# Kernel tuning notes

Measured on AMD Instinct MI355X. Metric: run time of the kernel, lower is better.

## Reference

```python
import jax, jax.numpy as jnp
import numpy as np

B, N, D, H, PSI = 8, 7225, 256, 8, 64
DH = D // H
DF = 4 * D
EPS = 1e-5


def _ln(x, g, b):
    m = jnp.mean(x, axis=-1, keepdims=True)
    v = jnp.mean((x - m) ** 2, axis=-1, keepdims=True)
    return (x - m) / jnp.sqrt(v + EPS) * g + b


def _gelu(x):
    return jax.nn.gelu(x, approximate=False)


def setup_inputs() -> dict:
    key = jax.random.key(0)
    ks = jax.random.split(key, 16)
    w = lambda k, s: (jax.random.normal(k, s, dtype=jnp.float32) * 0.02)
    inp = {
        'x': jax.random.normal(ks[0], (B, N, D), dtype=jnp.float32),
        'fx': jax.random.normal(ks[1], (B, N, D), dtype=jnp.float32),
        'ln1_g': jnp.ones((D,), jnp.float32), 'ln1_b': jnp.zeros((D,), jnp.float32),
        'Wq': w(ks[2], (D, D)), 'Wk': w(ks[3], (D, D)), 'Wv': w(ks[4], (D, D)),
        'Wo': w(ks[5], (D, D)), 'bo': jnp.zeros((D,), jnp.float32),
        'ln2_g': jnp.ones((D,), jnp.float32), 'ln2_b': jnp.zeros((D,), jnp.float32),
        'mlp_W1': w(ks[6], (D, DF)), 'mlp_b1': jnp.zeros((DF,), jnp.float32),
        'mlp_W2': w(ks[7], (DF, D)), 'mlp_b2': jnp.zeros((D,), jnp.float32),
        'proj_W1': w(ks[8], (D, D)), 'proj_b1': jnp.zeros((D,), jnp.float32),
        'proj_W2': w(ks[9], (D, PSI)), 'proj_b2': jnp.zeros((PSI,), jnp.float32),
        'mu': jnp.zeros((PSI,), jnp.float32),
        'ln3_g': jnp.ones((D,), jnp.float32), 'ln3_b': jnp.zeros((D,), jnp.float32),
        'mlp2_W1': w(ks[10], (D, DF)), 'mlp2_b1': jnp.zeros((DF,), jnp.float32),
        'mlp2_W2': w(ks[11], (DF, D)), 'mlp2_b2': jnp.zeros((D,), jnp.float32),
    }
    return inp


def _forward(x, fx, ln1_g, ln1_b, Wq, Wk, Wv, Wo, bo, ln2_g, ln2_b,
             mlp_W1, mlp_b1, mlp_W2, mlp_b2, proj_W1, proj_b1, proj_W2, proj_b2,
             mu, ln3_g, ln3_b, mlp2_W1, mlp2_b1, mlp2_W2, mlp2_b2):
    # --- linear (kernelized, non-causal) self-attention ---
    h = _ln(x, ln1_g, ln1_b)
    to_heads = lambda t: t.reshape(B, N, H, DH).transpose(0, 2, 1, 3)  # bhnd
    q = to_heads(h @ Wq)
    k = to_heads(h @ Wk)
    v = to_heads(h @ Wv)
    q = jax.nn.softmax(q, axis=-1) * (DH ** -0.5)   # feature-dim softmax
    k = jax.nn.softmax(k, axis=-2)                  # sequence-dim softmax
    ctx = jnp.einsum('bhnd,bhne->bhde', k, v)       # [B,H,DH,DH]
    attn = jnp.einsum('bhnd,bhde->bhne', q, ctx)    # [B,H,N,DH]
    attn = attn.transpose(0, 2, 1, 3).reshape(B, N, D) @ Wo + bo
    x = attn + x

    # --- MLP block (n_layers=0, no residual inside MLP) ---
    h = _ln(x, ln2_g, ln2_b)
    x = _gelu(h @ mlp_W1 + mlp_b1) @ mlp_W2 + mlp_b2 + x

    # --- low-rank projection + covariance whitening (orth=True, training path) ---
    x_ = _gelu(x @ proj_W1 + proj_b1) @ proj_W2 + proj_b2       # [B,N,PSI]
    cov = jnp.einsum('blc,bld->cd', x_, x_) / (B * N)           # [PSI,PSI]
    L = jnp.linalg.cholesky(cov)
    L_inv_T = jnp.linalg.inv(L).T
    x_ = x_ @ L_inv_T

    # --- softplus-scaled low-rank operator on fx ---
    ctx2 = jnp.einsum('blp,bld->bpd', x_, fx)                   # [B,PSI,D]
    fx = jnp.einsum('blp,bpd->bld', x_ * jax.nn.softplus(mu), ctx2)

    fx = _gelu(_ln(fx, ln3_g, ln3_b) @ mlp2_W1 + mlp2_b1) @ mlp2_W2 + mlp2_b2
    return x, fx


def reference(x, fx, ln1_g, ln1_b, Wq, Wk, Wv, Wo, bo, ln2_g, ln2_b,
              mlp_W1, mlp_b1, mlp_W2, mlp_b2, proj_W1, proj_b1, proj_W2, proj_b2,
              mu, ln3_g, ln3_b, mlp2_W1, mlp2_b1, mlp2_W2, mlp2_b2):
    return _forward(x, fx, ln1_g, ln1_b, Wq, Wk, Wv, Wo, bo, ln2_g, ln2_b,
                    mlp_W1, mlp_b1, mlp_W2, mlp_b2, proj_W1, proj_b1, proj_W2, proj_b2,
                    mu, ln3_g, ln3_b, mlp2_W1, mlp2_b1, mlp2_W2, mlp2_b2)
```

## Files before the change

kernel.cpp:

```cpp
#include <hip/hip_runtime.h>
#include <math.h>

typedef unsigned short u16;
typedef unsigned int u32;
typedef float f32x4 __attribute__((ext_vector_type(4)));
typedef __bf16 bf16x8 __attribute__((ext_vector_type(8)));

#define NTOK 57800
#define NSEQ 7225
#define NBATCH 8

static __device__ __forceinline__ float bf2f(u16 u){ u32 x=((u32)u)<<16; float f; __builtin_memcpy(&f,&x,4); return f; }
static __device__ __forceinline__ u16 f2bf(float f){ __bf16 h = (__bf16)f; u16 u; __builtin_memcpy(&u,&h,2); return u; }
static __device__ __forceinline__ float gelu_f(float v){
  float t = v * v;
  float w = fmaf(t, -0.07135481627f, -1.5957691216f);
  float e = __expf(w * v);
  return v * __builtin_amdgcn_rcpf(1.0f + e);
}

static __device__ __forceinline__ void gl16(const u16* g, u16* l){
  __builtin_amdgcn_global_load_lds((const __attribute__((address_space(1))) void*)g,
                                   (__attribute__((address_space(3))) void*)l, 16, 0, 0);
}

static __device__ __forceinline__ float rdlane(float v, int lane){
  int i; __builtin_memcpy(&i,&v,4);
  int r = __builtin_amdgcn_readlane(i, lane);
  float f; __builtin_memcpy(&f,&r,4);
  return f;
}

struct WJobs { const float* src[10]; u16* dst[10]; int K[10]; int N[10]; };
__global__ __launch_bounds__(256) void wtrans_all(WJobs j){
  int z = blockIdx.z;
  int K = j.K[z], N = j.N[z];
  int bk = blockIdx.x*32, bn = blockIdx.y*32;
  if (bk >= K || bn >= N) return;
  const float* src = j.src[z];
  u16* dst = j.dst[z];
  __shared__ float t[32][33];
  int tx = threadIdx.x&31, ty = threadIdx.x>>5;
  #pragma unroll
  for (int u=0;u<4;u++){
    int k = bk+ty+u*8, n = bn+tx;
    if (k<K && n<N) t[ty+u*8][tx] = src[(long)k*N+n];
  }
  __syncthreads();
  #pragma unroll
  for (int u=0;u<4;u++){
    int n = bn+ty+u*8, k = bk+tx;
    if (n<N && k<K) dst[(long)n*K+k] = f2bf(t[tx][ty+u*8]);
  }
}

__global__ __launch_bounds__(256) void ln_kernel(const float* __restrict__ in, const float* __restrict__ g,
                                                 const float* __restrict__ b, u16* __restrict__ out, int rows){
  int wid = threadIdx.x>>6, lane = threadIdx.x&63;
  int row = blockIdx.x*4 + wid;
  if (row >= rows) return;
  const float4 xv = *reinterpret_cast<const float4*>(in + (long)row*256 + lane*4);
  float s = xv.x+xv.y+xv.z+xv.w;
  float s2 = xv.x*xv.x+xv.y*xv.y+xv.z*xv.z+xv.w*xv.w;
  #pragma unroll
  for (int o=32;o;o>>=1){ s += __shfl_xor(s,o,64); s2 += __shfl_xor(s2,o,64); }
  float mean = s*(1.f/256.f);
  float var = fmaxf(s2*(1.f/256.f) - mean*mean, 0.f);
  float rstd = rsqrtf(var + 1e-5f);
  float4 gv = *reinterpret_cast<const float4*>(g + lane*4);
  float4 bv = *reinterpret_cast<const float4*>(b + lane*4);
  ushort4 o4;
  o4.x = f2bf((xv.x-mean)*rstd*gv.x + bv.x);
  o4.y = f2bf((xv.y-mean)*rstd*gv.y + bv.y);
  o4.z = f2bf((xv.z-mean)*rstd*gv.z + bv.z);
  o4.w = f2bf((xv.w-mean)*rstd*gv.w + bv.w);
  *reinterpret_cast<ushort4*>(out + (long)row*256 + lane*4) = o4;
}

template<bool BIASF, bool RESF, bool GELUF, bool OF32, bool OBF16>
__global__ __launch_bounds__(256) void gemm3(const u16* __restrict__ A, const u16* __restrict__ Bt,
    const float* __restrict__ bias, const float* __restrict__ resid,
    float* __restrict__ outF, u16* __restrict__ outB,
    int M, int N, int K, int gn, long aB, long bB, long cB)
{
  __shared__ __align__(16) u16 lds[2][2][8192];
  int nwg = gridDim.x, bid = blockIdx.x;
  int qx = nwg>>3, rx = nwg&7;
  int xcd = bid&7, lin = bid>>3;
  int swz = (xcd<rx)? (xcd*(qx+1)+lin) : (rx + xcd*qx + lin);
  int mi_ = swz/gn;
  int m0 = mi_*128, n0 = (swz - mi_*gn)*128;

  const u16* Ab  = A  + (long)blockIdx.z*aB;
  const u16* Btb = Bt + (long)blockIdx.z*bB;
  long coff = (long)blockIdx.z*cB;
  int tid = threadIdx.x, w = tid>>6, l = tid&63;
  int lr = l>>3;
  int csrc = (((l&7) ^ lr) << 3);
  int l15 = l&15, lq = l>>4;
  int wm = (w>>1)*64, wn = (w&1)*64;
  int sx = (l15&7)<<3;

  f32x4 acc[4][4];
  #pragma unroll
  for (int a=0;a<4;a++)
    #pragma unroll
    for (int b2=0;b2<4;b2++)
      #pragma unroll
      for (int r2=0;r2<4;r2++) acc[a][b2][r2]=0.f;

  int nt = K>>6;

  auto STAGE = [&](int k0, int bufi){
    #pragma unroll
    for (int u=0;u<4;u++){
      int rr = w*32 + u*8;
      gl16(Ab  + (long)(m0+rr+lr)*K + k0 + csrc, &lds[bufi][0][0] + rr*64 + l*8);
      gl16(Btb + (long)(n0+rr+lr)*K + k0 + csrc, &lds[bufi][1][0] + rr*64 + l*8);
    }
  };

  STAGE(0, 0);
  for (int t=0; t<nt; t++){
    int cur = t&1;
    asm volatile("s_waitcnt vmcnt(0)" ::: "memory");
    __builtin_amdgcn_s_barrier();
    asm volatile("" ::: "memory");
    if (t+1 < nt) STAGE((t+1)<<6, cur^1);
    asm volatile("" ::: "memory");
    #pragma unroll
    for (int ks=0;ks<2;ks++){
      bf16x8 af[4], bfv[4];
      int ko = ks*32 + lq*8;
      #pragma unroll
      for (int mi=0;mi<4;mi++)
        af[mi]  = *reinterpret_cast<const bf16x8*>(&lds[cur][0][0] + (wm+mi*16+l15)*64 + (ko ^ sx));
      #pragma unroll
      for (int ni=0;ni<4;ni++)
        bfv[ni] = *reinterpret_cast<const bf16x8*>(&lds[cur][1][0] + (wn+ni*16+l15)*64 + (ko ^ sx));
      #pragma unroll
      for (int mi=0;mi<4;mi++)
        #pragma unroll
        for (int ni=0;ni<4;ni++)
          acc[mi][ni] = __builtin_amdgcn_mfma_f32_16x16x32_bf16(bfv[ni], af[mi], acc[mi][ni], 0,0,0);
    }
  }

  #pragma unroll
  for (int mi=0;mi<4;mi++){
    int row = m0 + wm + mi*16 + l15;
    if (row >= M) continue;
    #pragma unroll
    for (int ni=0;ni<4;ni++){
      int col0 = n0 + wn + ni*16 + lq*4;
      if (col0 >= N) continue;
      f32x4 v = acc[mi][ni];
      if (BIASF){
        const float4 bv = *reinterpret_cast<const float4*>(bias + col0);
        v[0]+=bv.x; v[1]+=bv.y; v[2]+=bv.z; v[3]+=bv.w;
      }
      long idx = (long)row*N + col0;
      if (RESF){
        const float4 rv = *reinterpret_cast<const float4*>(resid + coff + idx);
        v[0]+=rv.x; v[1]+=rv.y; v[2]+=rv.z; v[3]+=rv.w;
      }
      if (GELUF){
        #pragma unroll
        for (int r2=0;r2<4;r2++) v[r2] = gelu_f(v[r2]);
      }
      if (OF32){
        float4 o; o.x=v[0]; o.y=v[1]; o.z=v[2]; o.w=v[3];
        *reinterpret_cast<float4*>(outF + coff + idx) = o;
      }
      if (OBF16){
        ushort4 o; o.x=f2bf(v[0]); o.y=f2bf(v[1]); o.z=f2bf(v[2]); o.w=f2bf(v[3]);
        *reinterpret_cast<ushort4*>(outB + coff + idx) = o;
      }
    }
  }
}

__global__ __launch_bounds__(256) void ctx_part(const u16* __restrict__ qkvb, float* __restrict__ part,
                                                float* __restrict__ spart2){
  int ch = blockIdx.x, bh = blockIdx.y; int b = bh>>3, h = bh&7;
  __shared__ float ek[8][32], vl[8][32];
  int tid = threadIdx.x;
  int d = tid&31, eg = (tid>>5)*4;
  float acc[4] = {0.f,0.f,0.f,0.f};
  float ssum = 0.f;
  int n0 = ch*226; int n1 = n0+226; if (n1 > NSEQ) n1 = NSEQ;
  for (int nb=n0; nb<n1; nb+=8){
    #pragma unroll
    for (int u=0;u<2;u++){
      int idx = tid + u*256; int r = idx>>6, c = idx&63;
      int n = nb + r;
      if (c < 32) ek[r][c]    = (n<n1)? __expf(bf2f(qkvb[((long)(b*NSEQ+n))*768 + 256 + h*32 + c])) : 0.f;
      else        vl[r][c-32] = (n<n1)? bf2f(qkvb[((long)(b*NSEQ+n))*768 + 512 + h*32 + (c-32)]) : 0.f;
    }
    __syncthreads();
    #pragma unroll
    for (int r=0;r<8;r++){
      float kv = ek[r][d];
      ssum += kv;
      #pragma unroll
      for (int j=0;j<4;j++) acc[j] += kv * vl[r][eg+j];
    }
    __syncthreads();
  }
  #pragma unroll
  for (int j=0;j<4;j++) part[((long)(bh*32+ch))*1024 + d*32 + eg + j] = acc[j];
  if (tid < 32) spart2[(bh*32+ch)*32 + d] = ssum;
}
__global__ void ctx_red(const float* __restrict__ part, const float* __restrict__ spart2,
                        float* __restrict__ ctx){
  int bh = blockIdx.x;
  __shared__ float sinvl[32];
  int tid = threadIdx.x;
  if (tid < 32){
    float s=0.f;
    for (int ch=0;ch<32;ch++) s += spart2[(bh*32+ch)*32 + tid];
    sinvl[tid] = 1.0f/s;
  }
  __syncthreads();
  for (int idx=tid; idx<1024; idx+=256){
    float s=0.f;
    for (int ch=0;ch<32;ch++) s += part[((long)(bh*32+ch))*1024 + idx];
    ctx[(long)bh*1024 + idx] = s * sinvl[idx>>5];
  }
}

__global__ __launch_bounds__(256) void qsoftmax(const u16* __restrict__ qkvb, u16* __restrict__ qsb){
  int wid = threadIdx.x>>6, lane = threadIdx.x&63;
  int n = blockIdx.x*4 + wid;
  int b = blockIdx.y;
  if (n >= NSEQ) return;
  const ushort4 qv = *reinterpret_cast<const ushort4*>(qkvb + ((long)(b*NSEQ+n))*768 + lane*4);
  float e0 = __expf(bf2f(qv.x)), e1 = __expf(bf2f(qv.y)),
        e2 = __expf(bf2f(qv.z)), e3 = __expf(bf2f(qv.w));
  float s = e0+e1+e2+e3;
  s += __shfl_xor(s,1,64); s += __shfl_xor(s,2,64); s += __shfl_xor(s,4,64);
  float r = 0.17677669529663687f / s;
  ushort4 o; o.x=f2bf(e0*r); o.y=f2bf(e1*r); o.z=f2bf(e2*r); o.w=f2bf(e3*r);
  *reinterpret_cast<ushort4*>(qsb + ((long)(b*NSEQ+n))*256 + lane*4) = o;
}

__global__ __launch_bounds__(256) void ctx_wo(const float* __restrict__ ctx, const u16* __restrict__ wot,
                                              u16* __restrict__ w2bt){
  int jg = blockIdx.x, b = blockIdx.y;
  int j0 = jg*32;
  __shared__ u16 wol[32][256];
  int tid = threadIdx.x;
  {
    int r = tid>>3, c = (tid&7)*32;
    const uint4* src = reinterpret_cast<const uint4*>(wot + (j0+r)*256 + c);
    uint4* dst = reinterpret_cast<uint4*>(&wol[r][c]);
    dst[0]=src[0]; dst[1]=src[1]; dst[2]=src[2]; dst[3]=src[3];
  }
  int h = tid>>5, d = tid&31;
  float creg[32];
  {
    const float4* cp = reinterpret_cast<const float4*>(ctx + (long)(b*8+h)*1024 + d*32);
    #pragma unroll
    for (int u=0;u<8;u++){ float4 v = cp[u]; creg[u*4]=v.x; creg[u*4+1]=v.y; creg[u*4+2]=v.z; creg[u*4+3]=v.w; }
  }
  __syncthreads();
  for (int jj=0;jj<32;jj++){
    const uint4* wp = reinterpret_cast<const uint4*>(&wol[jj][h*32]);
    float acc = 0.f;
    #pragma unroll
    for (int u=0;u<4;u++){
      uint4 wv = wp[u];
      acc += bf2f((u16)(wv.x&0xffffu))*creg[u*8+0] + bf2f((u16)(wv.x>>16))*creg[u*8+1]
           + bf2f((u16)(wv.y&0xffffu))*creg[u*8+2] + bf2f((u16)(wv.y>>16))*creg[u*8+3]
           + bf2f((u16)(wv.z&0xffffu))*creg[u*8+4] + bf2f((u16)(wv.z>>16))*creg[u*8+5]
           + bf2f((u16)(wv.w&0xffffu))*creg[u*8+6] + bf2f((u16)(wv.w>>16))*creg[u*8+7];
    }
    w2bt[((long)b*256 + j0+jj)*256 + tid] = f2bf(acc);
  }
}

__global__ __launch_bounds__(256) void cov_part(const float* __restrict__ xu, float* __restrict__ part){
  int ch = blockIdx.x;
  __shared__ float xl[2][8][64];
  int tid = threadIdx.x;
  int i = tid&63, jg = (tid>>6)*16;
  int lrow = tid>>5, lcol = (tid&31)*2;
  float acc[16];
  #pragma unroll
  for (int j=0;j<16;j++) acc[j]=0.f;
  int n0 = ch*113;
  const int NT = 15;
  float2 xr2;
  auto LOAD = [&](int t){
    int n = n0 + t*8 + lrow;
    if (n < n0+113 && n < NTOK) xr2 = *reinterpret_cast<const float2*>(xu + (long)n*64 + lcol);
    else { xr2.x = 0.f; xr2.y = 0.f; }
  };
  LOAD(0);
  for (int t=0; t<NT; t++){
    int cur = t&1;
    xl[cur][lrow][lcol] = xr2.x; xl[cur][lrow][lcol+1] = xr2.y;
    __syncthreads();
    if (t+1 < NT) LOAD(t+1);
    #pragma unroll
    for (int r=0;r<8;r++){
      float xv = xl[cur][r][i];
      const float4* fb = reinterpret_cast<const float4*>(&xl[cur][r][jg]);
      float4 f0=fb[0], f1=fb[1], f2=fb[2], f3=fb[3];
      acc[0]+=xv*f0.x; acc[1]+=xv*f0.y; acc[2]+=xv*f0.z; acc[3]+=xv*f0.w;
      acc[4]+=xv*f1.x; acc[5]+=xv*f1.y; acc[6]+=xv*f1.z; acc[7]+=xv*f1.w;
      acc[8]+=xv*f2.x; acc[9]+=xv*f2.y; acc[10]+=xv*f2.z; acc[11]+=xv*f2.w;
      acc[12]+=xv*f3.x; acc[13]+=xv*f3.y; acc[14]+=xv*f3.z; acc[15]+=xv*f3.w;
    }
    __syncthreads();
  }
  #pragma unroll
  for (int j=0;j<16;j++) part[(long)ch*4096 + (jg+j)*64 + i] = acc[j];
}
__global__ void cov_red(const float* __restrict__ part, float* __restrict__ cov){
  __shared__ float red[4][64];
  int o = blockIdx.x*64 + (threadIdx.x&63);
  int sl = threadIdx.x>>6;
  float s=0.f;
  for (int ch=sl; ch<512; ch+=4) s += part[(long)ch*4096 + o];
  if (sl>0) red[sl][threadIdx.x&63] = s;
  __syncthreads();
  if (sl==0){
    s += red[1][threadIdx.x&63] + red[2][threadIdx.x&63] + red[3][threadIdx.x&63];
    cov[o] = s * (1.0f/57800.0f);
  }
}

__global__ __launch_bounds__(64) void chol_inv(const float* __restrict__ cov, float* __restrict__ Linv){
  int t = threadIdx.x;
  float r[64];
  #pragma unroll
  for (int k=0;k<16;k++){
    float4 v4 = *reinterpret_cast<const float4*>(cov + (long)t*64 + k*4);
    r[k*4]=v4.x; r[k*4+1]=v4.y; r[k*4+2]=v4.z; r[k*4+3]=v4.w;
  }
  float dinv[64];
  #pragma unroll
  for (int j=0;j<64;j++){
    float ajj = rdlane(r[j], j);
    float ljj = sqrtf(fmaxf(ajj, 1e-20f));
    float rinv = 1.0f / ljj;
    dinv[j] = rinv;
    float ltj = r[j] * rinv;
    r[j] = ltj;
    #pragma unroll
    for (int k=j+1;k<64;k++){
      float lkj = rdlane(ltj, k);
      r[k] -= ltj * lkj;
    }
  }
  float v[64];
  #pragma unroll
  for (int k=0;k<64;k++) v[k] = (k==t) ? 1.f : 0.f;
  #pragma unroll
  for (int i=0;i<64;i++){
    float xi = v[i] * dinv[i];
    Linv[i*64 + t] = xi;
    #pragma unroll
    for (int k=i+1;k<64;k++){
      v[k] -= rdlane(r[i], k) * xi;
    }
  }
}

__global__ __launch_bounds__(256) void whiten(const float* __restrict__ xu, const float* __restrict__ Linv,
                                              const float* __restrict__ mu, u16* __restrict__ xw, u16* __restrict__ xws){
  __shared__ float Ll[64][65];
  int tid = threadIdx.x;
  for (int u=0; u<16; u++){ int idx = u*256+tid; Ll[idx>>6][idx&63] = Linv[idx]; }
  __syncthreads();
  int wid = tid>>6, lane = tid&63;
  float m = mu[lane];
  float sp = (m > 20.f)? m : log1pf(expf(m));
  for (int rr=0; rr<4; rr++){
    int row = blockIdx.x*16 + wid*4 + rr;
    if (row >= NTOK) continue;
    float xj = xu[(long)row*64 + lane];
    float s = 0.f;
    #pragma unroll
    for (int j=0;j<64;j++) s += __shfl(xj, j, 64) * Ll[lane][j];
    xw[(long)row*64+lane]  = f2bf(s);
    xws[(long)row*64+lane] = f2bf(s * sp);
  }
}

__global__ __launch_bounds__(256) void ctx2_part(const u16* __restrict__ xw, const float* __restrict__ fx,
                                                 float* __restrict__ part){
  int ch = blockIdx.x, b = blockIdx.y;
  __shared__ float xwlf[2][8][64];
  __shared__ float fxl[2][8][256];
  int tid = threadIdx.x;
  int p = tid&63, jg = (tid>>6)*64;
  int lrow = tid>>5, lcol = (tid&31)*8, xcol = (tid&31)*2;
  float acc[64];
  #pragma unroll
  for (int j=0;j<64;j++) acc[j]=0.f;
  int n0 = ch*226;
  int n1 = n0+226; if (n1 > NSEQ) n1 = NSEQ;
  const int NT = 29;
  float4 fra, frb; u32 xr;
  auto LOAD = [&](int t){
    int n = n0 + t*8 + lrow;
    if (n < n1){
      const float4* fp = reinterpret_cast<const float4*>(fx + ((long)b*NSEQ+n)*256 + lcol);
      fra = fp[0]; frb = fp[1];
      xr = *reinterpret_cast<const u32*>(xw + ((long)b*NSEQ+n)*64 + xcol);
    } else {
      fra.x=0.f; fra.y=0.f; fra.z=0.f; fra.w=0.f;
      frb.x=0.f; frb.y=0.f; frb.z=0.f; frb.w=0.f;
      xr = 0;
    }
  };
  LOAD(0);
  for (int t=0; t<NT; t++){
    int cur = t&1;
    xwlf[cur][lrow][xcol]   = bf2f((u16)(xr&0xffffu));
    xwlf[cur][lrow][xcol+1] = bf2f((u16)(xr>>16));
    *reinterpret_cast<float4*>(&fxl[cur][lrow][lcol])   = fra;
    *reinterpret_cast<float4*>(&fxl[cur][lrow][lcol+4]) = frb;
    __syncthreads();
    if (t+1 < NT) LOAD(t+1);
    #pragma unroll
    for (int r=0;r<8;r++){
      float xv = xwlf[cur][r][p];
      const float4* fb = reinterpret_cast<const float4*>(&fxl[cur][r][jg]);
      #pragma unroll
      for (int c4=0;c4<16;c4++){
        float4 f = fb[c4];
        acc[c4*4+0]+=xv*f.x; acc[c4*4+1]+=xv*f.y; acc[c4*4+2]+=xv*f.z; acc[c4*4+3]+=xv*f.w;
      }
    }
    __syncthreads();
  }
  long base = ((long)(b*32+ch)*256 + jg)*64 + p;
  #pragma unroll
  for (int j=0;j<64;j++) part[base + (long)j*64] = acc[j];
}
__global__ void ctx2_red(const float* __restrict__ part, u16* __restrict__ c2t){
  int b = blockIdx.y;
  int idx0 = blockIdx.x*1024 + threadIdx.x;
  #pragma unroll
  for (int u=0;u<4;u++){
    int id = idx0 + u*256;
    float s=0.f;
    for (int ch=0;ch<32;ch++) s += part[(long)(b*32+ch)*16384 + id];
    c2t[(long)b*16384 + id] = f2bf(s);
  }
}

extern "C" void kernel_launch(void* const* d_in, const int* in_sizes, int n_in,
                              void* d_out, int out_size, void* d_ws, size_t ws_size,
                              hipStream_t stream)
{
  (void)in_sizes; (void)n_in; (void)out_size; (void)ws_size;
  const float* x     = (const float*)d_in[0];
  const float* fx    = (const float*)d_in[1];
  const float* ln1_g = (const float*)d_in[2];
  const float* ln1_b = (const float*)d_in[3];
  const float* Wq    = (const float*)d_in[4];
  const float* Wk    = (const float*)d_in[5];
  const float* Wv    = (const float*)d_in[6];
  const float* Wo    = (const float*)d_in[7];
  const float* bo    = (const float*)d_in[8];
  const float* ln2_g = (const float*)d_in[9];
  const float* ln2_b = (const float*)d_in[10];
  const float* mW1   = (const float*)d_in[11];
  const float* mb1   = (const float*)d_in[12];
  const float* mW2   = (const float*)d_in[13];
  const float* mb2   = (const float*)d_in[14];
  const float* pW1   = (const float*)d_in[15];
  const float* pb1   = (const float*)d_in[16];
  const float* pW2   = (const float*)d_in[17];
  const float* pb2   = (const float*)d_in[18];
  const float* mu    = (const float*)d_in[19];
  const float* ln3_g = (const float*)d_in[20];
  const float* ln3_b = (const float*)d_in[21];
  const float* m2W1  = (const float*)d_in[22];
  const float* m2b1  = (const float*)d_in[23];
  const float* m2W2  = (const float*)d_in[24];
  const float* m2b2  = (const float*)d_in[25];

  char* wsb = (char*)d_ws;
  u16* wt    = (u16*)wsb;
  u16* WQKVT = wt + 0;
  u16* WOT   = wt + 196608;
  u16* W1T   = wt + 262144;
  u16* W2T   = wt + 524288;
  u16* PW1T  = wt + 786432;
  u16* PW2T  = wt + 851968;
  u16* M2W1T = wt + 884736;
  u16* M2W2T = wt + 1146880;

  constexpr size_t OFF_H      = 2818048;
  constexpr size_t OFF_QKV    = 32440320;
  constexpr size_t OFF_ATT    = 150929408;
  constexpr size_t OFF_SPART2 = 180551680;
  constexpr size_t OFF_XU     = 180813824;
  constexpr size_t OFF_CTXP   = OFF_XU;
  constexpr size_t OFF_CTX    = OFF_XU + 8388608;
  constexpr size_t OFF_XW     = 195624960;
  constexpr size_t OFF_XWS    = 203023360;
  constexpr size_t OFF_W2BT   = 210430976;
  constexpr size_t OFF_COVP   = OFF_H;
  constexpr size_t OFF_COV    = OFF_H + 8388608;
  constexpr size_t OFF_LINV   = OFF_H + 8404992;
  constexpr size_t OFF_C2P    = OFF_QKV;
  constexpr size_t OFF_C2T    = OFF_QKV + 16777216;

  u16* h     = (u16*)(wsb + OFF_H);
  u16* qkvb  = (u16*)(wsb + OFF_QKV);
  u16* m1    = qkvb;
  u16* attb  = (u16*)(wsb + OFF_ATT);
  u16* qsb   = (u16*)(wsb + OFF_ATT);
  float* spart2= (float*)(wsb + OFF_SPART2);
  float* ctxp  = (float*)(wsb + OFF_CTXP);
  float* ctxb  = (float*)(wsb + OFF_CTX);
  float* xu    = (float*)(wsb + OFF_XU);
  u16*  xwb    = (u16*)(wsb + OFF_XW);
  u16*  xwsb   = (u16*)(wsb + OFF_XWS);
  float* covp  = (float*)(wsb + OFF_COVP);
  float* cov   = (float*)(wsb + OFF_COV);
  float* Linv  = (float*)(wsb + OFF_LINV);
  float* c2p   = (float*)(wsb + OFF_C2P);
  u16*  c2t    = (u16*)(wsb + OFF_C2T);
  u16*  w2bt   = (u16*)(wsb + OFF_W2BT);

  float* outx  = (float*)d_out;
  float* outfx = outx + 14796800;

  WJobs wj;
  wj.src[0]=Wq;   wj.dst[0]=WQKVT;          wj.K[0]=256;  wj.N[0]=256;
  wj.src[1]=Wk;   wj.dst[1]=WQKVT+65536;    wj.K[1]=256;  wj.N[1]=256;
  wj.src[2]=Wv;   wj.dst[2]=WQKVT+131072;   wj.K[2]=256;  wj.N[2]=256;
  wj.src[3]=Wo;   wj.dst[3]=WOT;            wj.K[3]=256;  wj.N[3]=256;
  wj.src[4]=mW1;  wj.dst[4]=W1T;            wj.K[4]=256;  wj.N[4]=1024;
  wj.src[5]=mW2;  wj.dst[5]=W2T;            wj.K[5]=1024; wj.N[5]=256;
  wj.src[6]=pW1;  wj.dst[6]=PW1T;           wj.K[6]=256;  wj.N[6]=256;
  wj.src[7]=pW2;  wj.dst[7]=PW2T;           wj.K[7]=256;  wj.N[7]=64;
  wj.src[8]=m2W1; wj.dst[8]=M2W1T;          wj.K[8]=256;  wj.N[8]=1024;
  wj.src[9]=m2W2; wj.dst[9]=M2W2T;          wj.K[9]=1024; wj.N[9]=256;
  wtrans_all<<<dim3(32,32,10),256,0,stream>>>(wj);

  ln_kernel<<<14450,256,0,stream>>>(x, ln1_g, ln1_b, h, NTOK);
  gemm3<false,false,false,false,true><<<dim3(452*6,1,1),256,0,stream>>>(
      h, WQKVT, nullptr, nullptr, nullptr, qkvb, NTOK, 768, 256, 6, 0,0,0);
  qsoftmax<<<dim3(1807,8),256,0,stream>>>(qkvb, qsb);
  ctx_part<<<dim3(32,64),256,0,stream>>>(qkvb, ctxp, spart2);
  ctx_red<<<64,256,0,stream>>>(ctxp, spart2, ctxb);
  ctx_wo<<<dim3(8,8),256,0,stream>>>(ctxb, WOT, w2bt);
  gemm3<true,true,false,true,false><<<dim3(57*2,1,8),256,0,stream>>>(
      qsb, w2bt, bo, x, outx, nullptr, NSEQ, 256, 256, 2,
      (long)NSEQ*256, 256*256, (long)NSEQ*256);

  ln_kernel<<<14450,256,0,stream>>>(outx, ln2_g, ln2_b, h, NTOK);
  gemm3<true,false,true,false,true><<<dim3(452*8,1,1),256,0,stream>>>(
      h, W1T, mb1, nullptr, nullptr, m1, NTOK, 1024, 256, 8, 0,0,0);
  gemm3<true,true,false,true,true><<<dim3(452*2,1,1),256,0,stream>>>(
      m1, W2T, mb2, outx, outx, attb, NTOK, 256, 1024, 2, 0,0,0);

  gemm3<true,false,true,false,true><<<dim3(452*2,1,1),256,0,stream>>>(
      attb, PW1T, pb1, nullptr, nullptr, h, NTOK, 256, 256, 2, 0,0,0);
  gemm3<true,false,false,true,false><<<dim3(452,1,1),256,0,stream>>>(
      h, PW2T, pb2, nullptr, xu, nullptr, NTOK, 64, 256, 1, 0,0,0);

  cov_part<<<512,256,0,stream>>>(xu, covp);
  cov_red<<<64,256,0,stream>>>(covp, cov);
  chol_inv<<<1,64,0,stream>>>(cov, Linv);
  whiten<<<3613,256,0,stream>>>(xu, Linv, mu, xwb, xwsb);

  ctx2_part<<<dim3(32,8),256,0,stream>>>(xwb, fx, c2p);
  ctx2_red<<<dim3(16,8),256,0,stream>>>(c2p, c2t);
  gemm3<false,false,false,true,false><<<dim3(57*2,1,8),256,0,stream>>>(
      xwsb, c2t, nullptr, nullptr, outfx, nullptr, NSEQ, 256, 64, 2,
      (long)NSEQ*64, 256*64, (long)NSEQ*256);

  ln_kernel<<<14450,256,0,stream>>>(outfx, ln3_g, ln3_b, h, NTOK);
  gemm3<true,false,true,false,true><<<dim3(452*8,1,1),256,0,stream>>>(
      h, M2W1T, m2b1, nullptr, nullptr, m1, NTOK, 1024, 256, 8, 0,0,0);
  gemm3<true,false,false,true,false><<<dim3(452*2,1,1),256,0,stream>>>(
      m1, M2W2T, m2b2, nullptr, outfx, nullptr, NTOK, 256, 1024, 2, 0,0,0);
}
```

Measured before the change: 830.0 us.

## Fuse MLP up/down projections into one kernel keeping GELU activations in LDS

Adds an mlp_fused kernel that computes GELU(h@W1+b1)@W2+b2 per 128-row tile, staging the 1024-wide intermediate in LDS chunks so it is never written to global memory. Both MLP blocks use it, replacing two GEMM launches each. The generic GEMM is also changed from a double-buffered LDS pipeline to a single buffer with barriers, cutting LDS use but losing load/compute overlap. The fused kernel reads weight fragments directly from global memory and runs only 452 large blocks, which risks low occupancy.

```diff
diff --git a/kernel.cpp b/kernel.cpp
--- a/kernel.cpp
+++ b/kernel.cpp
@@ -83,7 +83,7 @@
     float* __restrict__ outF, u16* __restrict__ outB,
     int M, int N, int K, int gn, long aB, long bB, long cB)
 {
-  __shared__ __align__(16) u16 lds[2][2][8192];
+  __shared__ __align__(16) u16 lds[2][8192];
   int nwg = gridDim.x, bid = blockIdx.x;
   int qx = nwg>>3, rx = nwg&7;
   int xcd = bid&7, lin = bid>>3;
@@ -111,39 +111,37 @@
 
   int nt = K>>6;
 
-  auto STAGE = [&](int k0, int bufi){
+  auto STAGE = [&](int k0){
     #pragma unroll
     for (int u=0;u<4;u++){
       int rr = w*32 + u*8;
-      gl16(Ab  + (long)(m0+rr+lr)*K + k0 + csrc, &lds[bufi][0][0] + rr*64 + l*8);
-      gl16(Btb + (long)(n0+rr+lr)*K + k0 + csrc, &lds[bufi][1][0] + rr*64 + l*8);
+      gl16(Ab  + (long)(m0+rr+lr)*K + k0 + csrc, &lds[0][0] + rr*64 + l*8);
+      gl16(Btb + (long)(n0+rr+lr)*K + k0 + csrc, &lds[1][0] + rr*64 + l*8);
     }
   };
 
-  STAGE(0, 0);
-  for (int t=0; t<nt; t++){
-    int cur = t&1;
-    asm volatile("s_waitcnt vmcnt(0)" ::: "memory");
-    __builtin_amdgcn_s_barrier();
-    asm volatile("" ::: "memory");
-    if (t+1 < nt) STAGE((t+1)<<6, cur^1);
-    asm volatile("" ::: "memory");
+  STAGE(0);
+  for (int t=0;;t++){
+    __syncthreads();
     #pragma unroll
     for (int ks=0;ks<2;ks++){
       bf16x8 af[4], bfv[4];
       int ko = ks*32 + lq*8;
       #pragma unroll
       for (int mi=0;mi<4;mi++)
-        af[mi]  = *reinterpret_cast<const bf16x8*>(&lds[cur][0][0] + (wm+mi*16+l15)*64 + (ko ^ sx));
+        af[mi]  = *reinterpret_cast<const bf16x8*>(&lds[0][0] + (wm+mi*16+l15)*64 + (ko ^ sx));
       #pragma unroll
       for (int ni=0;ni<4;ni++)
-        bfv[ni] = *reinterpret_cast<const bf16x8*>(&lds[cur][1][0] + (wn+ni*16+l15)*64 + (ko ^ sx));
+        bfv[ni] = *reinterpret_cast<const bf16x8*>(&lds[1][0] + (wn+ni*16+l15)*64 + (ko ^ sx));
       #pragma unroll
       for (int mi=0;mi<4;mi++)
         #pragma unroll
         for (int ni=0;ni<4;ni++)
           acc[mi][ni] = __builtin_amdgcn_mfma_f32_16x16x32_bf16(bfv[ni], af[mi], acc[mi][ni], 0,0,0);
     }
+    if (t+1 == nt) break;
+    __syncthreads();
+    STAGE((t+1)<<6);
   }
 
   #pragma unroll
@@ -175,6 +173,142 @@
       if (OBF16){
         ushort4 o; o.x=f2bf(v[0]); o.y=f2bf(v[1]); o.z=f2bf(v[2]); o.w=f2bf(v[3]);
         *reinterpret_cast<ushort4*>(outB + coff + idx) = o;
+      }
+    }
+  }
+}
+
+template<bool RESF, bool OBF16>
+__global__ __launch_bounds__(512) void mlp_fused(const u16* __restrict__ A,
+    const u16* __restrict__ W1t, const float* __restrict__ b1,
+    const u16* __restrict__ W2t, const float* __restrict__ b2,
+    const float* __restrict__ resid, float* __restrict__ outF, u16* __restrict__ outB, int M)
+{
+  __shared__ __align__(16) u16 hA[4][8192];
+  __shared__ __align__(16) u16 P[2][16384];
+  int nwg = gridDim.x, bid = blockIdx.x;
+  int qx = nwg>>3, rx = nwg&7;
+  int xcd = bid&7, lin = bid>>3;
+  int swz = (xcd<rx)? (xcd*(qx+1)+lin) : (rx + xcd*qx + lin);
+  int m0 = swz*128;
+
+  int tid = threadIdx.x, w = tid>>6, l = tid&63;
+  int lr = l>>3;
+  int csrc = (((l&7) ^ lr) << 3);
+  int l15 = l&15, lq = l>>4;
+  int sx = (l15&7)<<3;
+  int wm = (w>>2)*64;
+  int jn1 = (w&3)*32;
+  int nn2 = (w&3)*64;
+
+  #pragma unroll
+  for (int kc=0; kc<4; kc++){
+    #pragma unroll
+    for (int u=0; u<2; u++){
+      int rr = w*16 + u*8;
+      gl16(A + (long)(m0+rr+lr)*256 + kc*64 + csrc, &hA[kc][0] + rr*64 + l*8);
+    }
+  }
+
+  f32x4 acc2[4][4];
+  #pragma unroll
+  for (int a=0;a<4;a++)
+    #pragma unroll
+    for (int b_=0;b_<4;b_++)
+      #pragma unroll
+      for (int r=0;r<4;r++) acc2[a][b_][r]=0.f;
+
+  asm volatile("s_waitcnt vmcnt(0)" ::: "memory");
+  __syncthreads();
+
+  #pragma unroll 1
+  for (int jb=0; jb<8; jb++){
+    int pc = jb&1;
+    f32x4 acc1[4][2];
+    #pragma unroll
+    for (int a=0;a<4;a++)
+      #pragma unroll
+      for (int b_=0;b_<2;b_++)
+        #pragma unroll
+        for (int r=0;r<4;r++) acc1[a][b_][r]=0.f;
+    #pragma unroll
+    for (int kc=0;kc<4;kc++){
+      #pragma unroll
+      for (int ks=0;ks<2;ks++){
+        int ko = ks*32 + lq*8;
+        bf16x8 af[4], bfv[2];
+        #pragma unroll
+        for (int ni=0;ni<2;ni++){
+          int jrow = jb*128 + jn1 + ni*16 + l15;
+          bfv[ni] = *reinterpret_cast<const bf16x8*>(W1t + (long)jrow*256 + kc*64 + ko);
+        }
+        #pragma unroll
+        for (int mi=0;mi<4;mi++)
+          af[mi] = *reinterpret_cast<const bf16x8*>(&hA[kc][0] + (wm+mi*16+l15)*64 + (ko ^ sx));
+        #pragma unroll
+        for (int mi=0;mi<4;mi++)
+          #pragma unroll
+          for (int ni=0;ni<2;ni++)
+            acc1[mi][ni] = __builtin_amdgcn_mfma_f32_16x16x32_bf16(bfv[ni], af[mi], acc1[mi][ni], 0,0,0);
+      }
+    }
+    #pragma unroll
+    for (int mi=0;mi<4;mi++){
+      int row = wm + mi*16 + l15;
+      #pragma unroll
+      for (int ni=0;ni<2;ni++){
+        int jj = jn1 + ni*16 + lq*4;
+        const float4 bv = *reinterpret_cast<const float4*>(b1 + jb*128 + jj);
+        f32x4 v = acc1[mi][ni];
+        v[0] = gelu_f(v[0]+bv.x); v[1] = gelu_f(v[1]+bv.y);
+        v[2] = gelu_f(v[2]+bv.z); v[3] = gelu_f(v[3]+bv.w);
+        ushort4 o; o.x=f2bf(v[0]); o.y=f2bf(v[1]); o.z=f2bf(v[2]); o.w=f2bf(v[3]);
+        int c = jj & 63, ch = jj >> 6;
+        *reinterpret_cast<ushort4*>(&P[pc][0] + ch*8192 + row*64 + (c ^ ((row&7)<<3))) = o;
+      }
+    }
+    __syncthreads();
+    #pragma unroll
+    for (int kk=0;kk<4;kk++){
+      int ko = (kk&1)*32 + lq*8;
+      int ch = kk>>1;
+      bf16x8 af2[4], bf2v[4];
+      #pragma unroll
+      for (int ni=0;ni<4;ni++){
+        int nrow = nn2 + ni*16 + l15;
+        bf2v[ni] = *reinterpret_cast<const bf16x8*>(W2t + (long)nrow*1024 + jb*128 + kk*32 + lq*8);
+      }
+      #pragma unroll
+      for (int mi=0;mi<4;mi++)
+        af2[mi] = *reinterpret_cast<const bf16x8*>(&P[pc][0] + ch*8192 + (wm+mi*16+l15)*64 + (ko ^ sx));
+      #pragma unroll
+      for (int mi=0;mi<4;mi++)
+        #pragma unroll
+        for (int ni=0;ni<4;ni++)
+          acc2[mi][ni] = __builtin_amdgcn_mfma_f32_16x16x32_bf16(bf2v[ni], af2[mi], acc2[mi][ni], 0,0,0);
+    }
+  }
+
+  #pragma unroll
+  for (int mi=0;mi<4;mi++){
+    int row = m0 + wm + mi*16 + l15;
+    if (row >= M) continue;
+    #pragma unroll
+    for (int ni=0;ni<4;ni++){
+      int col = nn2 + ni*16 + lq*4;
+      f32x4 v = acc2[mi][ni];
+      const float4 bv = *reinterpret_cast<const float4*>(b2 + col);
+      v[0]+=bv.x; v[1]+=bv.y; v[2]+=bv.z; v[3]+=bv.w;
+      long idx = (long)row*256 + col;
+      if (RESF){
+        const float4 rv = *reinterpret_cast<const float4*>(resid + idx);
+        v[0]+=rv.x; v[1]+=rv.y; v[2]+=rv.z; v[3]+=rv.w;
+      }
+      float4 o; o.x=v[0]; o.y=v[1]; o.z=v[2]; o.w=v[3];
+      *reinterpret_cast<float4*>(outF + idx) = o;
+      if (OBF16){
+        ushort4 ob; ob.x=f2bf(v[0]); ob.y=f2bf(v[1]); ob.z=f2bf(v[2]); ob.w=f2bf(v[3]);
+        *reinterpret_cast<ushort4*>(outB + idx) = ob;
       }
     }
   }
@@ -514,7 +648,6 @@
 
   u16* h     = (u16*)(wsb + OFF_H);
   u16* qkvb  = (u16*)(wsb + OFF_QKV);
-  u16* m1    = qkvb;
   u16* attb  = (u16*)(wsb + OFF_ATT);
   u16* qsb   = (u16*)(wsb + OFF_ATT);
   float* spart2= (float*)(wsb + OFF_SPART2);
@@ -558,10 +691,7 @@
       (long)NSEQ*256, 256*256, (long)NSEQ*256);
 
   ln_kernel<<<14450,256,0,stream>>>(outx, ln2_g, ln2_b, h, NTOK);
-  gemm3<true,false,true,false,true><<<dim3(452*8,1,1),256,0,stream>>>(
-      h, W1T, mb1, nullptr, nullptr, m1, NTOK, 1024, 256, 8, 0,0,0);
-  gemm3<true,true,false,true,true><<<dim3(452*2,1,1),256,0,stream>>>(
-      m1, W2T, mb2, outx, outx, attb, NTOK, 256, 1024, 2, 0,0,0);
+  mlp_fused<true,true><<<452,512,0,stream>>>(h, W1T, mb1, W2T, mb2, outx, outx, attb, NTOK);
 
   gemm3<true,false,true,false,true><<<dim3(452*2,1,1),256,0,stream>>>(
       attb, PW1T, pb1, nullptr, nullptr, h, NTOK, 256, 256, 2, 0,0,0);
@@ -580,8 +710,5 @@
       (long)NSEQ*64, 256*64, (long)NSEQ*256);
 
   ln_kernel<<<14450,256,0,stream>>>(outfx, ln3_g, ln3_b, h, NTOK);
-  gemm3<true,false,true,false,true><<<dim3(452*8,1,1),256,0,stream>>>(
-      h, M2W1T, m2b1, nullptr, nullptr, m1, NTOK, 1024, 256, 8, 0,0,0);
-  gemm3<true,false,false,true,false><<<dim3(452*2,1,1),256,0,stream>>>(
-      m1, M2W2T, m2b2, nullptr, outfx, nullptr, NTOK, 256, 1024, 2, 0,0,0);
-}
+  mlp_fused<false,false><<<452,512,0,stream>>>(h, M2W1T, m2b1, M2W2T, m2b2, nullptr, outfx, nullptr, NTOK);
+}
```

Measured after the change: 900.9 us. 8.5% more time.
